# Performance work log

Measured on AMD Instinct MI355X. Metric: run time of the kernel, lower is better.

Reference implementation:

```python
import jax, jax.numpy as jnp
import numpy as np

KSIZE = 7      # gaussian kernel size (SecondMomentMatrixLayer default)
SIGMA = 5.0    # gaussian sigma (default)
ALPHA = 0.05   # corner response alpha (CornerResponseLayer default)


def _gaussian_kernel(ksize, sigma):
    ax = np.arange(ksize, dtype=np.float64) - ksize // 2
    g1 = np.exp(-(ax ** 2) / (2.0 * sigma ** 2))
    k2 = np.outer(g1, g1)
    return (k2 / k2.sum()).astype(np.float32)


def setup_inputs() -> dict:
    key = jax.random.key(0)
    x = jax.random.normal(key, (4, 1, 2048, 2048), dtype=jnp.float32)
    # Sobel filters (ImageGradientsLayer): out-channels [Ix, Iy], shape (2,1,3,3)
    sobel_kernel = jnp.array(
        [[[[-1.0, 0.0, 1.0], [-2.0, 0.0, 2.0], [-1.0, 0.0, 1.0]]],
         [[[-1.0, -2.0, -1.0], [0.0, 0.0, 0.0], [1.0, 2.0, 1.0]]]],
        dtype=jnp.float32)
    # Depthwise (groups=3) gaussian kernel, shape (3,1,7,7)
    g = jnp.asarray(_gaussian_kernel(KSIZE, SIGMA))
    gauss_kernel = jnp.tile(g[None, None], (3, 1, 1, 1))
    return {"x": x, "sobel_kernel": sobel_kernel, "gauss_kernel": gauss_kernel}


def _conv(x, k, pad, groups=1):
    # torch Conv2d is cross-correlation; so is lax.conv_general_dilated
    return jax.lax.conv_general_dilated(
        x, k, window_strides=(1, 1), padding=[(pad, pad), (pad, pad)],
        dimension_numbers=("NCHW", "OIHW", "NCHW"), feature_group_count=groups)


def reference(x, sobel_kernel, gauss_kernel):
    # 1) image gradients via Sobel: (N,1,H,W) -> (N,2,H,W)
    grads = _conv(x, sobel_kernel, pad=1)
    Ix, Iy = grads[:, 0], grads[:, 1]
    # 2) channel products: I_xx, I_yy, I_xy -> (N,3,H,W)
    prods = jnp.stack([Ix * Ix, Iy * Iy, Ix * Iy], axis=1)
    # 3) gaussian-weighted second moments (depthwise conv, groups=3)
    S = _conv(prods, gauss_kernel, pad=KSIZE // 2, groups=3)
    Sxx, Syy, Sxy = S[:, 0], S[:, 1], S[:, 2]
    # 4) corner response R = det - alpha * trace^2 -> (N,1,H,W)
    trace = Sxx + Syy
    R = (Sxx * Syy - Sxy * Sxy - ALPHA * trace * trace)[:, None]
    # 5) NMS: global-median threshold, 7x7 stride-1 maxpool, binarize, scale by R
    median = jnp.quantile(R, 0.5, method="lower")  # torch.median = lower median
    thr = jnp.where(R < median, jnp.float32(0.0), R)
    pooled = jax.lax.reduce_window(
        thr, -jnp.inf, jax.lax.max, window_dimensions=(1, 1, 7, 7),
        window_strides=(1, 1, 1, 1),
        padding=[(0, 0), (0, 0), (3, 3), (3, 3)])
    binarized = jnp.where(thr == pooled, jnp.float32(1.0), jnp.float32(0.0))
    return binarized * R
```

## Files before the change

### kernel.cpp

```cpp
#include <hip/hip_runtime.h>
#include <math.h>

constexpr int IMH = 2048, IMW = 2048, NB = 4;
constexpr int NPIX = NB * IMH * IMW;
constexpr unsigned KSEL = 8388607u;

__device__ __forceinline__ unsigned f2u(float f) {
    unsigned b = __float_as_uint(f);
    return (b & 0x80000000u) ? ~b : (b | 0x80000000u);
}

__device__ __forceinline__ void gauss7(float* a) {
    double g[7]; double s = 0.0;
    #pragma unroll
    for (int i = 0; i < 7; ++i) { double ax = (double)(i - 3); g[i] = exp(-ax * ax / 50.0); s += g[i]; }
    #pragma unroll
    for (int i = 0; i < 7; ++i) a[i] = (float)(g[i] / s);
}

__launch_bounds__(256, 2)
__global__ void harris_R(const float* __restrict__ x, float* __restrict__ Rout) {
    __shared__ float smem[5184 + 4900 + 4900 + 4480];
    float* SX  = smem;
    float* SIX = smem + 5184;
    float* SIY = SIX + 4900;
    float* STH = SIY + 4900;
    float* SP  = SX;

    const int tid = threadIdx.x;
    const int x0 = blockIdx.x * 64, y0 = blockIdx.y * 64, b = blockIdx.z;
    const float* xb = x + (size_t)b * IMH * IMW;

    for (int i = tid; i < 72 * 72; i += 256) {
        int r = i / 72, c = i - r * 72;
        int gy = y0 - 4 + r, gx = x0 - 4 + c;
        float v = 0.0f;
        if ((unsigned)gy < (unsigned)IMH && (unsigned)gx < (unsigned)IMW) v = xb[gy * IMW + gx];
        SX[i] = v;
    }
    __syncthreads();

    for (int i = tid; i < 70 * 70; i += 256) {
        int r = i / 70, c = i - r * 70;
        int gy = y0 - 3 + r, gx = x0 - 3 + c;
        float ix = 0.0f, iy = 0.0f;
        if ((unsigned)gy < (unsigned)IMH && (unsigned)gx < (unsigned)IMW) {
            const float* p = SX + r * 72 + c;
            float x00 = p[0],   x01 = p[1],   x02 = p[2];
            float x10 = p[72],                 x12 = p[74];
            float x20 = p[144], x21 = p[145], x22 = p[146];
            ix = (x02 + 2.0f * x12 + x22) - (x00 + 2.0f * x10 + x20);
            iy = (x20 + 2.0f * x21 + x22) - (x00 + 2.0f * x01 + x02);
        }
        SIX[i] = ix; SIY[i] = iy;
    }
    __syncthreads();

    float a[7]; gauss7(a);
    const int lx = tid & 63, rb = tid >> 6;
    float Sacc[3][16];

    #pragma unroll
    for (int ch = 0; ch < 3; ++ch) {
        for (int i = tid; i < 70 * 70; i += 256) {
            float ix = SIX[i], iy = SIY[i];
            SP[i] = (ch == 0) ? ix * ix : (ch == 1) ? iy * iy : ix * iy;
        }
        __syncthreads();
        for (int i = tid; i < 70 * 64; i += 256) {
            int r = i >> 6, c = i & 63;
            const float* p = SP + r * 70 + c;
            float s = 0.0f;
            #pragma unroll
            for (int d = 0; d < 7; ++d) s += a[d] * p[d];
            STH[i] = s;
        }
        __syncthreads();
        #pragma unroll
        for (int k = 0; k < 16; ++k) {
            int r = rb + 4 * k;
            float s = 0.0f;
            #pragma unroll
            for (int d = 0; d < 7; ++d) s += a[d] * STH[(r + d) * 64 + lx];
            Sacc[ch][k] = s;
        }
        __syncthreads();
    }

    float* Rb = Rout + (size_t)b * IMH * IMW;
    #pragma unroll
    for (int k = 0; k < 16; ++k) {
        int r = rb + 4 * k;
        float sxx = Sacc[0][k], syy = Sacc[1][k], sxy = Sacc[2][k];
        float tr = sxx + syy;
        float R = sxx * syy - sxy * sxy - 0.05f * tr * tr;
        Rb[(size_t)(y0 + r) * IMW + (x0 + lx)] = R;
    }
}

__global__ void zero_kernel(unsigned* __restrict__ p, int n, int kidx, unsigned kval) {
    int i = blockIdx.x * blockDim.x + threadIdx.x;
    if (i < n) p[i] = (i == kidx) ? kval : 0u;
}

__global__ void hist1_kernel(const float* __restrict__ R, unsigned* __restrict__ hist) {
    __shared__ unsigned lh[4096];
    for (int i = threadIdx.x; i < 4096; i += 256) lh[i] = 0u;
    __syncthreads();
    const float4* R4 = (const float4*)R;
    const int n4 = NPIX / 4;
    for (int i = blockIdx.x * 256 + threadIdx.x; i < n4; i += gridDim.x * 256) {
        float4 v = R4[i];
        atomicAdd(&lh[f2u(v.x) >> 20], 1u);
        atomicAdd(&lh[f2u(v.y) >> 20], 1u);
        atomicAdd(&lh[f2u(v.z) >> 20], 1u);
        atomicAdd(&lh[f2u(v.w) >> 20], 1u);
    }
    __syncthreads();
    for (int i = threadIdx.x; i < 4096; i += 256) { unsigned c = lh[i]; if (c) atomicAdd(&hist[i], c); }
}

__global__ void hist2_kernel(const float* __restrict__ R, unsigned* __restrict__ hist,
                             const unsigned* __restrict__ sel) {
    __shared__ unsigned lh[4096];
    for (int i = threadIdx.x; i < 4096; i += 256) lh[i] = 0u;
    __syncthreads();
    const unsigned pref = sel[1];
    const float4* R4 = (const float4*)R;
    const int n4 = NPIX / 4;
    for (int i = blockIdx.x * 256 + threadIdx.x; i < n4; i += gridDim.x * 256) {
        float4 v = R4[i];
        unsigned u;
        u = f2u(v.x); if ((u >> 20) == pref) atomicAdd(&lh[(u >> 8) & 0xFFFu], 1u);
        u = f2u(v.y); if ((u >> 20) == pref) atomicAdd(&lh[(u >> 8) & 0xFFFu], 1u);
        u = f2u(v.z); if ((u >> 20) == pref) atomicAdd(&lh[(u >> 8) & 0xFFFu], 1u);
        u = f2u(v.w); if ((u >> 20) == pref) atomicAdd(&lh[(u >> 8) & 0xFFFu], 1u);
    }
    __syncthreads();
    for (int i = threadIdx.x; i < 4096; i += 256) { unsigned c = lh[i]; if (c) atomicAdd(&hist[i], c); }
}

__global__ void hist3_kernel(const float* __restrict__ R, unsigned* __restrict__ hist,
                             const unsigned* __restrict__ sel) {
    __shared__ unsigned lh[256];
    if (threadIdx.x < 256) lh[threadIdx.x] = 0u;
    __syncthreads();
    const unsigned pref = sel[1];
    const float4* R4 = (const float4*)R;
    const int n4 = NPIX / 4;
    for (int i = blockIdx.x * 256 + threadIdx.x; i < n4; i += gridDim.x * 256) {
        float4 v = R4[i];
        unsigned u;
        u = f2u(v.x); if ((u >> 8) == pref) atomicAdd(&lh[u & 0xFFu], 1u);
        u = f2u(v.y); if ((u >> 8) == pref) atomicAdd(&lh[u & 0xFFu], 1u);
        u = f2u(v.z); if ((u >> 8) == pref) atomicAdd(&lh[u & 0xFFu], 1u);
        u = f2u(v.w); if ((u >> 8) == pref) atomicAdd(&lh[u & 0xFFu], 1u);
    }
    __syncthreads();
    { unsigned c = lh[threadIdx.x]; if (c) atomicAdd(&hist[threadIdx.x], c); }
}

__global__ void select_kernel(const unsigned* __restrict__ hist, unsigned* __restrict__ sel,
                              int nbins, int bits, int final_stage) {
    __shared__ unsigned part[256];
    const int t = threadIdx.x;
    const int bpt = nbins >> 8;
    const unsigned krem = sel[0];
    unsigned s = 0;
    for (int i = 0; i < bpt; ++i) s += hist[t * bpt + i];
    part[t] = s;
    __syncthreads();
    if (t == 0) {
        unsigned run = 0; int ch = 255;
        for (int i = 0; i < 256; ++i) { if (run + part[i] > krem) { ch = i; break; } run += part[i]; }
        int bsel = ch * bpt; unsigned r2 = run;
        for (int j = ch * bpt; j < (ch + 1) * bpt; ++j) {
            if (r2 + hist[j] > krem) { bsel = j; break; }
            r2 += hist[j];
        }
        sel[0] = krem - r2;
        unsigned pref = (sel[1] << bits) | (unsigned)bsel;
        sel[1] = pref;
        if (final_stage) {
            unsigned fb = (pref & 0x80000000u) ? (pref ^ 0x80000000u) : ~pref;
            ((float*)sel)[2] = __uint_as_float(fb);
        }
    }
}

__launch_bounds__(256, 4)
__global__ void harris_out(const float* __restrict__ R, const unsigned* __restrict__ sel,
                           float* __restrict__ out) {
    __shared__ float SR[70 * 72];
    __shared__ float SM[70 * 64];
    const float med = ((const float*)sel)[2];
    const int tid = threadIdx.x;
    const int x0 = blockIdx.x * 64, y0 = blockIdx.y * 64, b = blockIdx.z;
    const float* Rb = R + (size_t)b * IMH * IMW;

    for (int i = tid; i < 70 * 70; i += 256) {
        int r = i / 70, c = i - r * 70;
        int gy = y0 - 3 + r, gx = x0 - 3 + c;
        float v = -INFINITY;
        if ((unsigned)gy < (unsigned)IMH && (unsigned)gx < (unsigned)IMW) v = Rb[gy * IMW + gx];
        SR[r * 72 + c] = v;
    }
    __syncthreads();

    for (int i = tid; i < 70 * 64; i += 256) {
        int r = i >> 6, c = i & 63;
        const float* p = SR + r * 72 + c;
        float m = -INFINITY;
        #pragma unroll
        for (int d = 0; d < 7; ++d) {
            float v = p[d];
            float t = (v < med) ? ((v == -INFINITY) ? -INFINITY : 0.0f) : v;
            m = fmaxf(m, t);
        }
        SM[i] = m;
    }
    __syncthreads();

    const int lx = tid & 63, rb = tid >> 6;
    float* ob = out + (size_t)b * IMH * IMW;
    #pragma unroll
    for (int k = 0; k < 16; ++k) {
        int r = rb + 4 * k;
        float pooled = -INFINITY;
        #pragma unroll
        for (int d = 0; d < 7; ++d) pooled = fmaxf(pooled, SM[(r + d) * 64 + lx]);
        float v = SR[(r + 3) * 72 + (lx + 3)];
        float t = (v < med) ? 0.0f : v;
        ob[(size_t)(y0 + r) * IMW + (x0 + lx)] = (t == pooled) ? v : 0.0f;
    }
}

extern "C" void kernel_launch(void* const* d_in, const int* in_sizes, int n_in,
                              void* d_out, int out_size, void* d_ws, size_t ws_size,
                              hipStream_t stream) {
    const float* x = (const float*)d_in[0];
    float* out = (float*)d_out;

    const size_t needed = (size_t)NPIX * 4 + (4096 + 4096 + 256 + 8) * 4;
    if (ws_size < needed) return;
    float* R = (float*)d_ws;
    unsigned* hbase = (unsigned*)((char*)d_ws + (size_t)NPIX * 4);
    unsigned* h1 = hbase;
    unsigned* h2 = hbase + 4096;
    unsigned* h3 = hbase + 8192;
    unsigned* sel = hbase + 8448;

    zero_kernel<<<(8456 + 255) / 256, 256, 0, stream>>>(hbase, 8456, 8448, KSEL);

    dim3 tgrid(IMW / 64, IMH / 64, NB);
    harris_R<<<tgrid, 256, 0, stream>>>(x, R);

    hist1_kernel<<<2048, 256, 0, stream>>>(R, h1);
    select_kernel<<<1, 256, 0, stream>>>(h1, sel, 4096, 12, 0);
    hist2_kernel<<<2048, 256, 0, stream>>>(R, h2, sel);
    select_kernel<<<1, 256, 0, stream>>>(h2, sel, 4096, 12, 0);
    hist3_kernel<<<2048, 256, 0, stream>>>(R, h3, sel);
    select_kernel<<<1, 256, 0, stream>>>(h3, sel, 256, 8, 1);

    harris_out<<<tgrid, 256, 0, stream>>>(R, sel, out);
}
```

Baseline: 336.2 us.

## Fuse first histogram into R kernel, merge gaussian channels, parallelize median select

The R kernel now computes all three second-moment products in a single horizontal pass over interleaved Ix/Iy, replacing three per-channel passes. It also builds the first-level radix histogram in shared memory, which removes one full read of R by the separate hist1 kernel. Tiles shrink to 64x32 so more blocks fit per CU. The select kernel uses a parallel prefix scan instead of a serial loop, and the gaussian weights are hardcoded constants. The trade-off is more halo overhead from the smaller tiles, and shared-memory atomics contending inside the main compute kernel.

```diff
diff --git a/kernel.cpp b/kernel.cpp
--- a/kernel.cpp
+++ b/kernel.cpp
@@ -11,36 +11,40 @@
 }
 
 __device__ __forceinline__ void gauss7(float* a) {
-    double g[7]; double s = 0.0;
-    #pragma unroll
-    for (int i = 0; i < 7; ++i) { double ax = (double)(i - 3); g[i] = exp(-ax * ax / 50.0); s += g[i]; }
-    #pragma unroll
-    for (int i = 0; i < 7; ++i) a[i] = (float)(g[i] / s);
-}
-
-__launch_bounds__(256, 2)
-__global__ void harris_R(const float* __restrict__ x, float* __restrict__ Rout) {
-    __shared__ float smem[5184 + 4900 + 4900 + 4480];
-    float* SX  = smem;
-    float* SIX = smem + 5184;
-    float* SIY = SIX + 4900;
-    float* STH = SIY + 4900;
-    float* SP  = SX;
+    const double g0 = 0.8352702114112720;
+    const double g1 = 0.9231163463866358;
+    const double g2 = 0.9801986733067553;
+    const double s = 2.0 * (g0 + g1 + g2) + 1.0;
+    const double inv = 1.0 / s;
+    a[0] = a[6] = (float)(g0 * inv);
+    a[1] = a[5] = (float)(g1 * inv);
+    a[2] = a[4] = (float)(g2 * inv);
+    a[3] = (float)inv;
+}
+
+__launch_bounds__(256, 3)
+__global__ void harris_R(const float* __restrict__ x, float* __restrict__ Rout,
+                         unsigned* __restrict__ hist) {
+    __shared__ float smem[12616];
+    float* SX   = smem;
+    float* STH  = smem;
+    float* SIXY = smem + 7296;
+    unsigned* LH = (unsigned*)(smem + 7296);
 
     const int tid = threadIdx.x;
-    const int x0 = blockIdx.x * 64, y0 = blockIdx.y * 64, b = blockIdx.z;
+    const int x0 = blockIdx.x * 64, y0 = blockIdx.y * 32, b = blockIdx.z;
     const float* xb = x + (size_t)b * IMH * IMW;
 
-    for (int i = tid; i < 72 * 72; i += 256) {
+    for (int i = tid; i < 40 * 72; i += 256) {
         int r = i / 72, c = i - r * 72;
         int gy = y0 - 4 + r, gx = x0 - 4 + c;
         float v = 0.0f;
-        if ((unsigned)gy < (unsigned)IMH && (unsigned)gx < (unsigned)IMW) v = xb[gy * IMW + gx];
+        if ((unsigned)gy < (unsigned)IMH && (unsigned)gx < (unsigned)IMW) v = xb[(size_t)gy * IMW + gx];
         SX[i] = v;
     }
     __syncthreads();
 
-    for (int i = tid; i < 70 * 70; i += 256) {
+    for (int i = tid; i < 38 * 70; i += 256) {
         int r = i / 70, c = i - r * 70;
         int gy = y0 - 3 + r, gx = x0 - 3 + c;
         float ix = 0.0f, iy = 0.0f;
@@ -52,72 +56,63 @@
             ix = (x02 + 2.0f * x12 + x22) - (x00 + 2.0f * x10 + x20);
             iy = (x20 + 2.0f * x21 + x22) - (x00 + 2.0f * x01 + x02);
         }
-        SIX[i] = ix; SIY[i] = iy;
+        SIXY[r * 140 + c * 2]     = ix;
+        SIXY[r * 140 + c * 2 + 1] = iy;
     }
     __syncthreads();
 
     float a[7]; gauss7(a);
+
+    for (int i = tid; i < 38 * 64; i += 256) {
+        int r = i >> 6, c = i & 63;
+        const float* p = SIXY + r * 140 + c * 2;
+        float sxx = 0.f, syy = 0.f, sxy = 0.f;
+        #pragma unroll
+        for (int d = 0; d < 7; ++d) {
+            float ix = p[2 * d], iy = p[2 * d + 1];
+            float t = a[d] * ix;
+            sxx += t * ix;
+            sxy += t * iy;
+            syy += (a[d] * iy) * iy;
+        }
+        float* q = STH + r * 192 + c * 3;
+        q[0] = sxx; q[1] = syy; q[2] = sxy;
+    }
+    __syncthreads();
+
+    for (int i = tid; i < 4096; i += 256) LH[i] = 0u;
+
     const int lx = tid & 63, rb = tid >> 6;
-    float Sacc[3][16];
-
-    #pragma unroll
-    for (int ch = 0; ch < 3; ++ch) {
-        for (int i = tid; i < 70 * 70; i += 256) {
-            float ix = SIX[i], iy = SIY[i];
-            SP[i] = (ch == 0) ? ix * ix : (ch == 1) ? iy * iy : ix * iy;
-        }
-        __syncthreads();
-        for (int i = tid; i < 70 * 64; i += 256) {
-            int r = i >> 6, c = i & 63;
-            const float* p = SP + r * 70 + c;
-            float s = 0.0f;
-            #pragma unroll
-            for (int d = 0; d < 7; ++d) s += a[d] * p[d];
-            STH[i] = s;
-        }
-        __syncthreads();
-        #pragma unroll
-        for (int k = 0; k < 16; ++k) {
-            int r = rb + 4 * k;
-            float s = 0.0f;
-            #pragma unroll
-            for (int d = 0; d < 7; ++d) s += a[d] * STH[(r + d) * 64 + lx];
-            Sacc[ch][k] = s;
-        }
-        __syncthreads();
-    }
-
     float* Rb = Rout + (size_t)b * IMH * IMW;
-    #pragma unroll
-    for (int k = 0; k < 16; ++k) {
-        int r = rb + 4 * k;
-        float sxx = Sacc[0][k], syy = Sacc[1][k], sxy = Sacc[2][k];
+    float rv[8];
+    #pragma unroll
+    for (int k = 0; k < 8; ++k) {
+        int ro = rb + 4 * k;
+        float sxx = 0.f, syy = 0.f, sxy = 0.f;
+        #pragma unroll
+        for (int d = 0; d < 7; ++d) {
+            const float* q = STH + (ro + d) * 192 + lx * 3;
+            sxx += a[d] * q[0];
+            syy += a[d] * q[1];
+            sxy += a[d] * q[2];
+        }
         float tr = sxx + syy;
         float R = sxx * syy - sxy * sxy - 0.05f * tr * tr;
-        Rb[(size_t)(y0 + r) * IMW + (x0 + lx)] = R;
-    }
+        rv[k] = R;
+        Rb[(size_t)(y0 + ro) * IMW + (x0 + lx)] = R;
+    }
+    __syncthreads();
+
+    #pragma unroll
+    for (int k = 0; k < 8; ++k) atomicAdd(&LH[f2u(rv[k]) >> 20], 1u);
+    __syncthreads();
+
+    for (int i = tid; i < 4096; i += 256) { unsigned c = LH[i]; if (c) atomicAdd(&hist[i], c); }
 }
 
 __global__ void zero_kernel(unsigned* __restrict__ p, int n, int kidx, unsigned kval) {
     int i = blockIdx.x * blockDim.x + threadIdx.x;
     if (i < n) p[i] = (i == kidx) ? kval : 0u;
-}
-
-__global__ void hist1_kernel(const float* __restrict__ R, unsigned* __restrict__ hist) {
-    __shared__ unsigned lh[4096];
-    for (int i = threadIdx.x; i < 4096; i += 256) lh[i] = 0u;
-    __syncthreads();
-    const float4* R4 = (const float4*)R;
-    const int n4 = NPIX / 4;
-    for (int i = blockIdx.x * 256 + threadIdx.x; i < n4; i += gridDim.x * 256) {
-        float4 v = R4[i];
-        atomicAdd(&lh[f2u(v.x) >> 20], 1u);
-        atomicAdd(&lh[f2u(v.y) >> 20], 1u);
-        atomicAdd(&lh[f2u(v.z) >> 20], 1u);
-        atomicAdd(&lh[f2u(v.w) >> 20], 1u);
-    }
-    __syncthreads();
-    for (int i = threadIdx.x; i < 4096; i += 256) { unsigned c = lh[i]; if (c) atomicAdd(&hist[i], c); }
 }
 
 __global__ void hist2_kernel(const float* __restrict__ R, unsigned* __restrict__ hist,
@@ -161,22 +156,37 @@
 }
 
 __global__ void select_kernel(const unsigned* __restrict__ hist, unsigned* __restrict__ sel,
-                              int nbins, int bits, int final_stage) {
+                              int bpt, int bits, int final_stage) {
     __shared__ unsigned part[256];
+    __shared__ unsigned grp[16];
+    __shared__ int chs;
+    __shared__ unsigned runs;
     const int t = threadIdx.x;
-    const int bpt = nbins >> 8;
     const unsigned krem = sel[0];
     unsigned s = 0;
     for (int i = 0; i < bpt; ++i) s += hist[t * bpt + i];
     part[t] = s;
     __syncthreads();
+    #pragma unroll
+    for (int off = 1; off < 256; off <<= 1) {
+        unsigned add = (t >= off) ? part[t - off] : 0u;
+        __syncthreads();
+        part[t] += add;
+        __syncthreads();
+    }
+    unsigned incl = part[t];
+    unsigned excl = incl - s;
+    if (excl <= krem && krem < incl) { chs = t; runs = excl; }
+    __syncthreads();
+    int ch = chs;
+    if (t < bpt) grp[t] = hist[ch * bpt + t];
+    __syncthreads();
     if (t == 0) {
-        unsigned run = 0; int ch = 255;
-        for (int i = 0; i < 256; ++i) { if (run + part[i] > krem) { ch = i; break; } run += part[i]; }
-        int bsel = ch * bpt; unsigned r2 = run;
-        for (int j = ch * bpt; j < (ch + 1) * bpt; ++j) {
-            if (r2 + hist[j] > krem) { bsel = j; break; }
-            r2 += hist[j];
+        unsigned r2 = runs; int bsel = ch * bpt;
+        for (int j = 0; j < bpt; ++j) {
+            unsigned h = grp[j];
+            if (r2 + h > krem) { bsel = ch * bpt + j; break; }
+            r2 += h;
         }
         sel[0] = krem - r2;
         unsigned pref = (sel[1] << bits) | (unsigned)bsel;
@@ -188,26 +198,26 @@
     }
 }
 
-__launch_bounds__(256, 4)
+__launch_bounds__(256, 7)
 __global__ void harris_out(const float* __restrict__ R, const unsigned* __restrict__ sel,
                            float* __restrict__ out) {
-    __shared__ float SR[70 * 72];
-    __shared__ float SM[70 * 64];
+    __shared__ float SR[38 * 72];
+    __shared__ float SM[38 * 64];
     const float med = ((const float*)sel)[2];
     const int tid = threadIdx.x;
-    const int x0 = blockIdx.x * 64, y0 = blockIdx.y * 64, b = blockIdx.z;
+    const int x0 = blockIdx.x * 64, y0 = blockIdx.y * 32, b = blockIdx.z;
     const float* Rb = R + (size_t)b * IMH * IMW;
 
-    for (int i = tid; i < 70 * 70; i += 256) {
+    for (int i = tid; i < 38 * 70; i += 256) {
         int r = i / 70, c = i - r * 70;
         int gy = y0 - 3 + r, gx = x0 - 3 + c;
         float v = -INFINITY;
-        if ((unsigned)gy < (unsigned)IMH && (unsigned)gx < (unsigned)IMW) v = Rb[gy * IMW + gx];
+        if ((unsigned)gy < (unsigned)IMH && (unsigned)gx < (unsigned)IMW) v = Rb[(size_t)gy * IMW + gx];
         SR[r * 72 + c] = v;
     }
     __syncthreads();
 
-    for (int i = tid; i < 70 * 64; i += 256) {
+    for (int i = tid; i < 38 * 64; i += 256) {
         int r = i >> 6, c = i & 63;
         const float* p = SR + r * 72 + c;
         float m = -INFINITY;
@@ -224,7 +234,7 @@
     const int lx = tid & 63, rb = tid >> 6;
     float* ob = out + (size_t)b * IMH * IMW;
     #pragma unroll
-    for (int k = 0; k < 16; ++k) {
+    for (int k = 0; k < 8; ++k) {
         int r = rb + 4 * k;
         float pooled = -INFINITY;
         #pragma unroll
@@ -252,15 +262,14 @@
 
     zero_kernel<<<(8456 + 255) / 256, 256, 0, stream>>>(hbase, 8456, 8448, KSEL);
 
-    dim3 tgrid(IMW / 64, IMH / 64, NB);
-    harris_R<<<tgrid, 256, 0, stream>>>(x, R);
-
-    hist1_kernel<<<2048, 256, 0, stream>>>(R, h1);
-    select_kernel<<<1, 256, 0, stream>>>(h1, sel, 4096, 12, 0);
+    dim3 tgrid(IMW / 64, IMH / 32, NB);
+    harris_R<<<tgrid, 256, 0, stream>>>(x, R, h1);
+
+    select_kernel<<<1, 256, 0, stream>>>(h1, sel, 16, 12, 0);
     hist2_kernel<<<2048, 256, 0, stream>>>(R, h2, sel);
-    select_kernel<<<1, 256, 0, stream>>>(h2, sel, 4096, 12, 0);
+    select_kernel<<<1, 256, 0, stream>>>(h2, sel, 16, 12, 0);
     hist3_kernel<<<2048, 256, 0, stream>>>(R, h3, sel);
-    select_kernel<<<1, 256, 0, stream>>>(h3, sel, 256, 8, 1);
+    select_kernel<<<1, 256, 0, stream>>>(h3, sel, 1, 8, 1);
 
     harris_out<<<tgrid, 256, 0, stream>>>(R, sel, out);
 }
```

Result: faster. 286.5 us (-14.8%).
